# Kernel optimization log

Measured on AMD Instinct MI355X. Metric: run time of the kernel, lower is better.

## Reference

```python
import jax, jax.numpy as jnp
import numpy as np

N = 100000   # nodes
E = 1600000  # edges (avg degree 16)
D = 64       # feature dim (in_dim)


def setup_inputs() -> dict:
    key = jax.random.key(0)
    k1, k2, k3, k4, k5 = jax.random.split(key, 5)
    h = jax.random.normal(k1, (N, D), dtype=jnp.float32)
    dnorm = jax.random.uniform(k2, (N,), dtype=jnp.float32)  # deg^-1/2 proxy
    # xavier_normal_(gain=1.414) for Linear(2D, 1): std = gain*sqrt(2/(fan_in+fan_out))
    std = 1.414 * np.sqrt(2.0 / (2 * D + 1))
    gate_w = jax.random.normal(k3, (1, 2 * D), dtype=jnp.float32) * std
    gate_b = jnp.zeros((1,), dtype=jnp.float32)
    src = jax.random.randint(k4, (E,), 0, N, dtype=jnp.int32)
    dst = jax.random.randint(k5, (E,), 0, N, dtype=jnp.int32)
    return {"h": h, "dnorm": dnorm, "gate_w": gate_w, "gate_b": gate_b,
            "src": src, "dst": dst}


def reference(h, dnorm, gate_w, gate_b, src, dst):
    # gate(cat[h_dst, h_src]) == h_dst @ W[:, :D].T + h_src @ W[:, D:].T + b
    w_dst = gate_w[0, :D]  # [D]
    w_src = gate_w[0, D:]  # [D]
    h_src = h[src]                                        # [E, D] gather
    g = jnp.tanh(h[dst] @ w_dst + h_src @ w_src + gate_b[0])  # [E]
    e = g * dnorm[dst] * dnorm[src]                       # [E] (dropout p=0 -> identity)
    # u_mul_e + sum: z[v] = sum_{(u->v)} h[u] * e
    z = jax.ops.segment_sum(h_src * e[:, None], dst, num_segments=N)  # [N, D]
    return z
```

## Files before the change

### kernel.cpp

```cpp
#include <hip/hip_runtime.h>
#include <hip/hip_bf16.h>

#define D 64
#define BKT_SHIFT 7
#define BKT_NODES 128
#define NB_CNT 1024
#define DSPLIT_T 1024
#define DSPLIT_E 4096
#define CAP 2560

__device__ __forceinline__ unsigned short f2bf(float x) {
    unsigned u = __float_as_uint(x);
    unsigned r = 0x7fffu + ((u >> 16) & 1u);
    return (unsigned short)((u + r) >> 16);
}

template<bool MAKE_BF16>
__global__ void fal_precompute(const float* __restrict__ h,
                               const float* __restrict__ dnorm,
                               const float* __restrict__ gate_w,
                               const float* __restrict__ gate_b,
                               float2* __restrict__ sd,
                               float2* __restrict__ ss,
                               unsigned short* __restrict__ hb,
                               int N) {
    int tid  = threadIdx.x;
    int lane = tid & 63;
    int wave = tid >> 6;
    int grp  = lane >> 4;
    int gl   = lane & 15;

    int node = blockIdx.x * 16 + wave * 4 + grp;
    int nc   = node < N ? node : N - 1;

    const float4* h4 = (const float4*)h;
    const float4* w4 = (const float4*)gate_w;

    float4 hv  = h4[nc * 16 + gl];
    float4 wd  = w4[gl];
    float4 wsr = w4[16 + gl];

    if (MAKE_BF16 && node < N) {
        ushort4 p = make_ushort4(f2bf(hv.x), f2bf(hv.y), f2bf(hv.z), f2bf(hv.w));
        *(ushort4*)&hb[(size_t)node * D + gl * 4] = p;
    }

    float a = hv.x * wd.x + hv.y * wd.y + hv.z * wd.z + hv.w * wd.w;
    float b = hv.x * wsr.x + hv.y * wsr.y + hv.z * wsr.z + hv.w * wsr.w;

    for (int off = 1; off < 16; off <<= 1) {
        a += __shfl_xor(a, off, 64);
        b += __shfl_xor(b, off, 64);
    }

    if (gl == 0 && node < N) {
        float dn = dnorm[node];
        sd[node] = make_float2(a + gate_b[0], dn);
        ss[node] = make_float2(b, dn);
    }
}

__global__ __launch_bounds__(DSPLIT_T) void fal_multisplit(
        const int* __restrict__ src,
        const int* __restrict__ dst,
        int* __restrict__ bcursor,
        unsigned* __restrict__ pk_bin,
        int E, int nb) {
    __shared__ int lcount[NB_CNT];
    __shared__ int lscan[NB_CNT];
    __shared__ int gofs[NB_CNT];
    __shared__ int wsum16[16];
    __shared__ unsigned s_pk[DSPLIT_E];
    __shared__ int s_gpos[DSPLIT_E];

    int tid  = threadIdx.x;
    int lane = tid & 63;
    int w    = tid >> 6;
    lcount[tid] = 0;
    __syncthreads();

    int E4 = E >> 2;
    int i4 = blockIdx.x * DSPLIT_T + tid;

    int srcs[4], dsts[4], lr[4];
    bool act = (i4 < E4);
    if (act) {
        int4 s4 = ((const int4*)src)[i4];
        int4 d4 = ((const int4*)dst)[i4];
        srcs[0] = s4.x; srcs[1] = s4.y; srcs[2] = s4.z; srcs[3] = s4.w;
        dsts[0] = d4.x; dsts[1] = d4.y; dsts[2] = d4.z; dsts[3] = d4.w;
        #pragma unroll
        for (int j = 0; j < 4; ++j)
            lr[j] = atomicAdd(&lcount[dsts[j] >> BKT_SHIFT], 1);
    }
    __syncthreads();

    int v = lcount[tid];
    for (int off = 1; off < 64; off <<= 1) {
        int t = __shfl_up(v, off, 64);
        if (lane >= off) v += t;
    }
    if (lane == 63) wsum16[w] = v;
    __syncthreads();
    if (tid < 16) {
        int s = wsum16[tid];
        for (int off = 1; off < 16; off <<= 1) {
            int t = __shfl_up(s, off, 64);
            if (tid >= off) s += t;
        }
        wsum16[tid] = s;
    }
    __syncthreads();
    lscan[tid] = v + (w ? wsum16[w - 1] : 0);

    if (tid < nb) {
        int c = lcount[tid];
        int rel = c ? atomicAdd(&bcursor[tid], c) : 0;
        gofs[tid] = tid * CAP + rel;
    }
    __syncthreads();

    if (act) {
        #pragma unroll
        for (int j = 0; j < 4; ++j) {
            int b = dsts[j] >> BKT_SHIFT;
            int lpos = (lscan[b] - lcount[b]) + lr[j];
            unsigned dl = (unsigned)(dsts[j] & (BKT_NODES - 1));
            s_pk[lpos] = (dl << 20) | (unsigned)srcs[j];
            int gp = gofs[b] + lr[j];
            s_gpos[lpos] = (gp < (b + 1) * CAP) ? gp : -1;
        }
    }
    __syncthreads();

    int total = lscan[NB_CNT - 1];
    for (int t = tid; t < total; t += DSPLIT_T) {
        int g = s_gpos[t];
        if (g >= 0) pk_bin[g] = s_pk[t];
    }
}

template<bool BF16>
__global__ __launch_bounds__(512) void fal_bucket_process(
        const float* __restrict__ h,
        const unsigned short* __restrict__ hb,
        const float2* __restrict__ sd,
        const float2* __restrict__ ss,
        const int* __restrict__ bcursor,
        const unsigned* __restrict__ pk_bin,
        float* __restrict__ z, int N) {
    __shared__ unsigned s_pk[CAP];
    __shared__ unsigned s_srt[CAP];
    __shared__ float    s_esc[CAP];
    __shared__ float2   sdl[BKT_NODES];
    __shared__ int nhist[BKT_NODES];
    __shared__ int nbase[BKT_NODES];
    __shared__ int ncur[BKT_NODES];
    __shared__ int wsum8[8];

    int b    = blockIdx.x;
    int tid  = threadIdx.x;
    int lane = tid & 63;
    int w    = tid >> 6;

    if (tid < BKT_NODES) {
        nhist[tid] = 0;
        int node = b * BKT_NODES + tid;
        sdl[tid] = (node < N) ? sd[node] : make_float2(0.f, 0.f);
    }
    __syncthreads();

    int cnt = min(bcursor[b], CAP);
    const unsigned* bin = pk_bin + (size_t)b * CAP;

    for (int t = tid; t < cnt; t += 512) {
        unsigned pk = bin[t];
        s_pk[t] = pk;
        atomicAdd(&nhist[pk >> 20], 1);
    }
    __syncthreads();

    int myh = (tid < BKT_NODES) ? nhist[tid] : 0;
    int v = myh;
    for (int off = 1; off < 64; off <<= 1) {
        int t = __shfl_up(v, off, 64);
        if (lane >= off) v += t;
    }
    if (lane == 63) wsum8[w] = v;
    __syncthreads();
    if (tid < 8) {
        int s2 = wsum8[tid];
        for (int off = 1; off < 8; off <<= 1) {
            int t = __shfl_up(s2, off, 64);
            if (tid >= off) s2 += t;
        }
        wsum8[tid] = s2;
    }
    __syncthreads();
    if (tid < BKT_NODES) {
        int incl = v + (w ? wsum8[w - 1] : 0);
        nbase[tid] = incl - myh;
        ncur[tid]  = 0;
    }
    __syncthreads();

    for (int t = tid; t < cnt; t += 512) {
        unsigned pk = s_pk[t];
        int dl = (int)(pk >> 20);
        int sn = (int)(pk & 0xFFFFFu);
        int r  = atomicAdd(&ncur[dl], 1);
        float2 sv = ss[sn];
        float2 dv = sdl[dl];
        float esc = tanhf(dv.x + sv.x) * dv.y * sv.y;
        int p = nbase[dl] + r;
        s_srt[p] = pk;
        s_esc[p] = esc;
    }
    __syncthreads();

    int oct  = tid >> 3;
    int sdim = tid & 7;

    #pragma unroll
    for (int ni = 0; ni < BKT_NODES / 64; ++ni) {
        int dl   = oct + ni * 64;
        int seg0 = nbase[dl];
        int dg   = nhist[dl];

        float acc[8];
        #pragma unroll
        for (int i = 0; i < 8; ++i) acc[i] = 0.0f;

        int k = 0;
        for (; k + 2 <= dg; k += 2) {
            unsigned p0 = s_srt[seg0 + k];
            unsigned p1 = s_srt[seg0 + k + 1];
            float    e0 = s_esc[seg0 + k];
            float    e1 = s_esc[seg0 + k + 1];
            int s0 = (int)(p0 & 0xFFFFFu);
            int s1 = (int)(p1 & 0xFFFFFu);
            if (BF16) {
                uint4 a0 = *(const uint4*)&hb[(size_t)s0 * D + sdim * 8];
                uint4 a1 = *(const uint4*)&hb[(size_t)s1 * D + sdim * 8];
                acc[0] = fmaf(__uint_as_float(a0.x << 16),         e0, acc[0]);
                acc[1] = fmaf(__uint_as_float(a0.x & 0xffff0000u), e0, acc[1]);
                acc[2] = fmaf(__uint_as_float(a0.y << 16),         e0, acc[2]);
                acc[3] = fmaf(__uint_as_float(a0.y & 0xffff0000u), e0, acc[3]);
                acc[4] = fmaf(__uint_as_float(a0.z << 16),         e0, acc[4]);
                acc[5] = fmaf(__uint_as_float(a0.z & 0xffff0000u), e0, acc[5]);
                acc[6] = fmaf(__uint_as_float(a0.w << 16),         e0, acc[6]);
                acc[7] = fmaf(__uint_as_float(a0.w & 0xffff0000u), e0, acc[7]);
                acc[0] = fmaf(__uint_as_float(a1.x << 16),         e1, acc[0]);
                acc[1] = fmaf(__uint_as_float(a1.x & 0xffff0000u), e1, acc[1]);
                acc[2] = fmaf(__uint_as_float(a1.y << 16),         e1, acc[2]);
                acc[3] = fmaf(__uint_as_float(a1.y & 0xffff0000u), e1, acc[3]);
                acc[4] = fmaf(__uint_as_float(a1.z << 16),         e1, acc[4]);
                acc[5] = fmaf(__uint_as_float(a1.z & 0xffff0000u), e1, acc[5]);
                acc[6] = fmaf(__uint_as_float(a1.w << 16),         e1, acc[6]);
                acc[7] = fmaf(__uint_as_float(a1.w & 0xffff0000u), e1, acc[7]);
            } else {
                const float4* hp0 = (const float4*)&h[(size_t)s0 * D + sdim * 8];
                const float4* hp1 = (const float4*)&h[(size_t)s1 * D + sdim * 8];
                float4 q0 = hp0[0], q1 = hp0[1], q2 = hp1[0], q3 = hp1[1];
                acc[0] = fmaf(q0.x, e0, acc[0]); acc[1] = fmaf(q0.y, e0, acc[1]);
                acc[2] = fmaf(q0.z, e0, acc[2]); acc[3] = fmaf(q0.w, e0, acc[3]);
                acc[4] = fmaf(q1.x, e0, acc[4]); acc[5] = fmaf(q1.y, e0, acc[5]);
                acc[6] = fmaf(q1.z, e0, acc[6]); acc[7] = fmaf(q1.w, e0, acc[7]);
                acc[0] = fmaf(q2.x, e1, acc[0]); acc[1] = fmaf(q2.y, e1, acc[1]);
                acc[2] = fmaf(q2.z, e1, acc[2]); acc[3] = fmaf(q2.w, e1, acc[3]);
                acc[4] = fmaf(q3.x, e1, acc[4]); acc[5] = fmaf(q3.y, e1, acc[5]);
                acc[6] = fmaf(q3.z, e1, acc[6]); acc[7] = fmaf(q3.w, e1, acc[7]);
            }
        }
        if (k < dg) {
            unsigned p0 = s_srt[seg0 + k];
            float    e0 = s_esc[seg0 + k];
            int s0 = (int)(p0 & 0xFFFFFu);
            if (BF16) {
                uint4 a0 = *(const uint4*)&hb[(size_t)s0 * D + sdim * 8];
                acc[0] = fmaf(__uint_as_float(a0.x << 16),         e0, acc[0]);
                acc[1] = fmaf(__uint_as_float(a0.x & 0xffff0000u), e0, acc[1]);
                acc[2] = fmaf(__uint_as_float(a0.y << 16),         e0, acc[2]);
                acc[3] = fmaf(__uint_as_float(a0.y & 0xffff0000u), e0, acc[3]);
                acc[4] = fmaf(__uint_as_float(a0.z << 16),         e0, acc[4]);
                acc[5] = fmaf(__uint_as_float(a0.z & 0xffff0000u), e0, acc[5]);
                acc[6] = fmaf(__uint_as_float(a0.w << 16),         e0, acc[6]);
                acc[7] = fmaf(__uint_as_float(a0.w & 0xffff0000u), e0, acc[7]);
            } else {
                const float4* hp0 = (const float4*)&h[(size_t)s0 * D + sdim * 8];
                float4 q0 = hp0[0], q1 = hp0[1];
                acc[0] = fmaf(q0.x, e0, acc[0]); acc[1] = fmaf(q0.y, e0, acc[1]);
                acc[2] = fmaf(q0.z, e0, acc[2]); acc[3] = fmaf(q0.w, e0, acc[3]);
                acc[4] = fmaf(q1.x, e0, acc[4]); acc[5] = fmaf(q1.y, e0, acc[5]);
                acc[6] = fmaf(q1.z, e0, acc[6]); acc[7] = fmaf(q1.w, e0, acc[7]);
            }
        }

        int node = b * BKT_NODES + dl;
        if (node < N) {
            float4* zp = (float4*)&z[(size_t)node * D + sdim * 8];
            zp[0] = make_float4(acc[0], acc[1], acc[2], acc[3]);
            zp[1] = make_float4(acc[4], acc[5], acc[6], acc[7]);
        }
    }
}

extern "C" void kernel_launch(void* const* d_in, const int* in_sizes, int n_in,
                              void* d_out, int out_size, void* d_ws, size_t ws_size,
                              hipStream_t stream) {
    const float* h      = (const float*)d_in[0];
    const float* dnorm  = (const float*)d_in[1];
    const float* gate_w = (const float*)d_in[2];
    const float* gate_b = (const float*)d_in[3];
    const int*   src    = (const int*)d_in[4];
    const int*   dst    = (const int*)d_in[5];
    float*       z      = (float*)d_out;

    int N  = in_sizes[1];
    int E  = in_sizes[4];
    int nb = (N + BKT_NODES - 1) >> BKT_SHIFT;

    char* ws0 = (char*)d_ws;
    size_t off = 0;
    auto alloc = [&](size_t bytes) {
        char* p = ws0 + off;
        off += (bytes + 15) & ~(size_t)15;
        return p;
    };
    float2*   sd      = (float2*)alloc((size_t)N * sizeof(float2));
    float2*   ss      = (float2*)alloc((size_t)N * sizeof(float2));
    int*      bcursor = (int*)alloc((size_t)nb * sizeof(int));
    unsigned* pk_bin  = (unsigned*)alloc((size_t)nb * CAP * sizeof(unsigned));
    unsigned short* hb = (unsigned short*)(ws0 + off);
    size_t need_with_hb = off + (size_t)N * D * sizeof(unsigned short);
    bool use_bf16 = (ws_size >= need_with_hb);

    hipMemsetAsync(bcursor, 0, (size_t)nb * sizeof(int), stream);

    if (use_bf16)
        fal_precompute<true><<<(N + 15) / 16, 256, 0, stream>>>(
            h, dnorm, gate_w, gate_b, sd, ss, hb, N);
    else
        fal_precompute<false><<<(N + 15) / 16, 256, 0, stream>>>(
            h, dnorm, gate_w, gate_b, sd, ss, hb, N);

    fal_multisplit<<<(E + DSPLIT_E - 1) / DSPLIT_E, DSPLIT_T, 0, stream>>>(
        src, dst, bcursor, pk_bin, E, nb);

    if (use_bf16)
        fal_bucket_process<true><<<nb, 512, 0, stream>>>(
            h, hb, sd, ss, bcursor, pk_bin, z, N);
    else
        fal_bucket_process<false><<<nb, 512, 0, stream>>>(
            h, hb, sd, ss, bcursor, pk_bin, z, N);
}
```

Measured before the change: 169.7 us.

## Make bucket processing persistent with atomic work queue, pack sorted edges, unroll by four

```diff
diff --git a/kernel.cpp b/kernel.cpp
--- a/kernel.cpp
+++ b/kernel.cpp
@@ -148,160 +148,196 @@
         const float2* __restrict__ ss,
         const int* __restrict__ bcursor,
         const unsigned* __restrict__ pk_bin,
-        float* __restrict__ z, int N) {
+        int* __restrict__ wcur,
+        float* __restrict__ z, int N, int nb) {
     __shared__ unsigned s_pk[CAP];
-    __shared__ unsigned s_srt[CAP];
-    __shared__ float    s_esc[CAP];
+    __shared__ uint2    s_sorted[CAP];
     __shared__ float2   sdl[BKT_NODES];
     __shared__ int nhist[BKT_NODES];
     __shared__ int nbase[BKT_NODES];
     __shared__ int ncur[BKT_NODES];
     __shared__ int wsum8[8];
-
-    int b    = blockIdx.x;
+    __shared__ int s_b;
+
     int tid  = threadIdx.x;
     int lane = tid & 63;
     int w    = tid >> 6;
-
-    if (tid < BKT_NODES) {
-        nhist[tid] = 0;
-        int node = b * BKT_NODES + tid;
-        sdl[tid] = (node < N) ? sd[node] : make_float2(0.f, 0.f);
-    }
-    __syncthreads();
-
-    int cnt = min(bcursor[b], CAP);
-    const unsigned* bin = pk_bin + (size_t)b * CAP;
-
-    for (int t = tid; t < cnt; t += 512) {
-        unsigned pk = bin[t];
-        s_pk[t] = pk;
-        atomicAdd(&nhist[pk >> 20], 1);
-    }
-    __syncthreads();
-
-    int myh = (tid < BKT_NODES) ? nhist[tid] : 0;
-    int v = myh;
-    for (int off = 1; off < 64; off <<= 1) {
-        int t = __shfl_up(v, off, 64);
-        if (lane >= off) v += t;
-    }
-    if (lane == 63) wsum8[w] = v;
-    __syncthreads();
-    if (tid < 8) {
-        int s2 = wsum8[tid];
-        for (int off = 1; off < 8; off <<= 1) {
-            int t = __shfl_up(s2, off, 64);
-            if (tid >= off) s2 += t;
-        }
-        wsum8[tid] = s2;
-    }
-    __syncthreads();
-    if (tid < BKT_NODES) {
-        int incl = v + (w ? wsum8[w - 1] : 0);
-        nbase[tid] = incl - myh;
-        ncur[tid]  = 0;
-    }
-    __syncthreads();
-
-    for (int t = tid; t < cnt; t += 512) {
-        unsigned pk = s_pk[t];
-        int dl = (int)(pk >> 20);
-        int sn = (int)(pk & 0xFFFFFu);
-        int r  = atomicAdd(&ncur[dl], 1);
-        float2 sv = ss[sn];
-        float2 dv = sdl[dl];
-        float esc = tanhf(dv.x + sv.x) * dv.y * sv.y;
-        int p = nbase[dl] + r;
-        s_srt[p] = pk;
-        s_esc[p] = esc;
-    }
-    __syncthreads();
-
     int oct  = tid >> 3;
     int sdim = tid & 7;
 
-    #pragma unroll
-    for (int ni = 0; ni < BKT_NODES / 64; ++ni) {
-        int dl   = oct + ni * 64;
-        int seg0 = nbase[dl];
-        int dg   = nhist[dl];
-
-        float acc[8];
+    for (;;) {
+        if (tid == 0) s_b = atomicAdd(wcur, 1);
+        __syncthreads();
+        int b = s_b;
+        if (b >= nb) return;
+
+        if (tid < BKT_NODES) {
+            nhist[tid] = 0;
+            int node = b * BKT_NODES + tid;
+            sdl[tid] = (node < N) ? sd[node] : make_float2(0.f, 0.f);
+        }
+        __syncthreads();
+
+        int cnt = min(bcursor[b], CAP);
+        const unsigned* bin = pk_bin + (size_t)b * CAP;
+
+        for (int t = tid; t < cnt; t += 512) {
+            unsigned pk = bin[t];
+            s_pk[t] = pk;
+            atomicAdd(&nhist[pk >> 20], 1);
+        }
+        __syncthreads();
+
+        int myh = (tid < BKT_NODES) ? nhist[tid] : 0;
+        int v = myh;
+        for (int off = 1; off < 64; off <<= 1) {
+            int t = __shfl_up(v, off, 64);
+            if (lane >= off) v += t;
+        }
+        if (lane == 63) wsum8[w] = v;
+        __syncthreads();
+        if (tid < 8) {
+            int s2 = wsum8[tid];
+            for (int off = 1; off < 8; off <<= 1) {
+                int t = __shfl_up(s2, off, 64);
+                if (tid >= off) s2 += t;
+            }
+            wsum8[tid] = s2;
+        }
+        __syncthreads();
+        if (tid < BKT_NODES) {
+            int incl = v + (w ? wsum8[w - 1] : 0);
+            nbase[tid] = incl - myh;
+            ncur[tid]  = 0;
+        }
+        __syncthreads();
+
+        for (int t = tid; t < cnt; t += 512) {
+            unsigned pk = s_pk[t];
+            int dl = (int)(pk >> 20);
+            int sn = (int)(pk & 0xFFFFFu);
+            int r  = atomicAdd(&ncur[dl], 1);
+            float2 sv = ss[sn];
+            float2 dv = sdl[dl];
+            float esc = tanhf(dv.x + sv.x) * dv.y * sv.y;
+            s_sorted[nbase[dl] + r] = make_uint2(pk, __float_as_uint(esc));
+        }
+        __syncthreads();
+
         #pragma unroll
-        for (int i = 0; i < 8; ++i) acc[i] = 0.0f;
-
-        int k = 0;
-        for (; k + 2 <= dg; k += 2) {
-            unsigned p0 = s_srt[seg0 + k];
-            unsigned p1 = s_srt[seg0 + k + 1];
-            float    e0 = s_esc[seg0 + k];
-            float    e1 = s_esc[seg0 + k + 1];
-            int s0 = (int)(p0 & 0xFFFFFu);
-            int s1 = (int)(p1 & 0xFFFFFu);
-            if (BF16) {
-                uint4 a0 = *(const uint4*)&hb[(size_t)s0 * D + sdim * 8];
-                uint4 a1 = *(const uint4*)&hb[(size_t)s1 * D + sdim * 8];
-                acc[0] = fmaf(__uint_as_float(a0.x << 16),         e0, acc[0]);
-                acc[1] = fmaf(__uint_as_float(a0.x & 0xffff0000u), e0, acc[1]);
-                acc[2] = fmaf(__uint_as_float(a0.y << 16),         e0, acc[2]);
-                acc[3] = fmaf(__uint_as_float(a0.y & 0xffff0000u), e0, acc[3]);
-                acc[4] = fmaf(__uint_as_float(a0.z << 16),         e0, acc[4]);
-                acc[5] = fmaf(__uint_as_float(a0.z & 0xffff0000u), e0, acc[5]);
-                acc[6] = fmaf(__uint_as_float(a0.w << 16),         e0, acc[6]);
-                acc[7] = fmaf(__uint_as_float(a0.w & 0xffff0000u), e0, acc[7]);
-                acc[0] = fmaf(__uint_as_float(a1.x << 16),         e1, acc[0]);
-                acc[1] = fmaf(__uint_as_float(a1.x & 0xffff0000u), e1, acc[1]);
-                acc[2] = fmaf(__uint_as_float(a1.y << 16),         e1, acc[2]);
-                acc[3] = fmaf(__uint_as_float(a1.y & 0xffff0000u), e1, acc[3]);
-                acc[4] = fmaf(__uint_as_float(a1.z << 16),         e1, acc[4]);
-                acc[5] = fmaf(__uint_as_float(a1.z & 0xffff0000u), e1, acc[5]);
-                acc[6] = fmaf(__uint_as_float(a1.w << 16),         e1, acc[6]);
-                acc[7] = fmaf(__uint_as_float(a1.w & 0xffff0000u), e1, acc[7]);
-            } else {
-                const float4* hp0 = (const float4*)&h[(size_t)s0 * D + sdim * 8];
-                const float4* hp1 = (const float4*)&h[(size_t)s1 * D + sdim * 8];
-                float4 q0 = hp0[0], q1 = hp0[1], q2 = hp1[0], q3 = hp1[1];
-                acc[0] = fmaf(q0.x, e0, acc[0]); acc[1] = fmaf(q0.y, e0, acc[1]);
-                acc[2] = fmaf(q0.z, e0, acc[2]); acc[3] = fmaf(q0.w, e0, acc[3]);
-                acc[4] = fmaf(q1.x, e0, acc[4]); acc[5] = fmaf(q1.y, e0, acc[5]);
-                acc[6] = fmaf(q1.z, e0, acc[6]); acc[7] = fmaf(q1.w, e0, acc[7]);
-                acc[0] = fmaf(q2.x, e1, acc[0]); acc[1] = fmaf(q2.y, e1, acc[1]);
-                acc[2] = fmaf(q2.z, e1, acc[2]); acc[3] = fmaf(q2.w, e1, acc[3]);
-                acc[4] = fmaf(q3.x, e1, acc[4]); acc[5] = fmaf(q3.y, e1, acc[5]);
-                acc[6] = fmaf(q3.z, e1, acc[6]); acc[7] = fmaf(q3.w, e1, acc[7]);
+        for (int ni = 0; ni < BKT_NODES / 64; ++ni) {
+            int dl   = oct + ni * 64;
+            int seg0 = nbase[dl];
+            int dg   = nhist[dl];
+
+            float acc[8];
+            #pragma unroll
+            for (int i = 0; i < 8; ++i) acc[i] = 0.0f;
+
+            int k = 0;
+            for (; k + 4 <= dg; k += 4) {
+                uint2 r0 = s_sorted[seg0 + k];
+                uint2 r1 = s_sorted[seg0 + k + 1];
+                uint2 r2 = s_sorted[seg0 + k + 2];
+                uint2 r3 = s_sorted[seg0 + k + 3];
+                int s0 = (int)(r0.x & 0xFFFFFu), s1 = (int)(r1.x & 0xFFFFFu);
+                int s2 = (int)(r2.x & 0xFFFFFu), s3 = (int)(r3.x & 0xFFFFFu);
+                float e0 = __uint_as_float(r0.y), e1 = __uint_as_float(r1.y);
+                float e2 = __uint_as_float(r2.y), e3 = __uint_as_float(r3.y);
+                if (BF16) {
+                    uint4 a0 = *(const uint4*)&hb[(size_t)s0 * D + sdim * 8];
+                    uint4 a1 = *(const uint4*)&hb[(size_t)s1 * D + sdim * 8];
+                    uint4 a2 = *(const uint4*)&hb[(size_t)s2 * D + sdim * 8];
+                    uint4 a3 = *(const uint4*)&hb[(size_t)s3 * D + sdim * 8];
+                    acc[0] = fmaf(__uint_as_float(a0.x << 16),         e0, acc[0]);
+                    acc[1] = fmaf(__uint_as_float(a0.x & 0xffff0000u), e0, acc[1]);
+                    acc[2] = fmaf(__uint_as_float(a0.y << 16),         e0, acc[2]);
+                    acc[3] = fmaf(__uint_as_float(a0.y & 0xffff0000u), e0, acc[3]);
+                    acc[4] = fmaf(__uint_as_float(a0.z << 16),         e0, acc[4]);
+                    acc[5] = fmaf(__uint_as_float(a0.z & 0xffff0000u), e0, acc[5]);
+                    acc[6] = fmaf(__uint_as_float(a0.w << 16),         e0, acc[6]);
+                    acc[7] = fmaf(__uint_as_float(a0.w & 0xffff0000u), e0, acc[7]);
+                    acc[0] = fmaf(__uint_as_float(a1.x << 16),         e1, acc[0]);
+                    acc[1] = fmaf(__uint_as_float(a1.x & 0xffff0000u), e1, acc[1]);
+                    acc[2] = fmaf(__uint_as_float(a1.y << 16),         e1, acc[2]);
+                    acc[3] = fmaf(__uint_as_float(a1.y & 0xffff0000u), e1, acc[3]);
+                    acc[4] = fmaf(__uint_as_float(a1.z << 16),         e1, acc[4]);
+                    acc[5] = fmaf(__uint_as_float(a1.z & 0xffff0000u), e1, acc[5]);
+                    acc[6] = fmaf(__uint_as_float(a1.w << 16),         e1, acc[6]);
+                    acc[7] = fmaf(__uint_as_float(a1.w & 0xffff0000u), e1, acc[7]);
+                    acc[0] = fmaf(__uint_as_float(a2.x << 16),         e2, acc[0]);
+                    acc[1] = fmaf(__uint_as_float(a2.x & 0xffff0000u), e2, acc[1]);
+                    acc[2] = fmaf(__uint_as_float(a2.y << 16),         e2, acc[2]);
+                    acc[3] = fmaf(__uint_as_float(a2.y & 0xffff0000u), e2, acc[3]);
+                    acc[4] = fmaf(__uint_as_float(a2.z << 16),         e2, acc[4]);
+                    acc[5] = fmaf(__uint_as_float(a2.z & 0xffff0000u), e2, acc[5]);
+                    acc[6] = fmaf(__uint_as_float(a2.w << 16),         e2, acc[6]);
+                    acc[7] = fmaf(__uint_as_float(a2.w & 0xffff0000u), e2, acc[7]);
+                    acc[0] = fmaf(__uint_as_float(a3.x << 16),         e3, acc[0]);
+                    acc[1] = fmaf(__uint_as_float(a3.x & 0xffff0000u), e3, acc[1]);
+                    acc[2] = fmaf(__uint_as_float(a3.y << 16),         e3, acc[2]);
+                    acc[3] = fmaf(__uint_as_float(a3.y & 0xffff0000u), e3, acc[3]);
+                    acc[4] = fmaf(__uint_as_float(a3.z << 16),         e3, acc[4]);
+                    acc[5] = fmaf(__uint_as_float(a3.z & 0xffff0000u), e3, acc[5]);
+                    acc[6] = fmaf(__uint_as_float(a3.w << 16),         e3, acc[6]);
+                    acc[7] = fmaf(__uint_as_float(a3.w & 0xffff0000u), e3, acc[7]);
+                } else {
+                    const float4* p0 = (const float4*)&h[(size_t)s0 * D + sdim * 8];
+                    const float4* p1 = (const float4*)&h[(size_t)s1 * D + sdim * 8];
+                    const float4* p2 = (const float4*)&h[(size_t)s2 * D + sdim * 8];
+                    const float4* p3 = (const float4*)&h[(size_t)s3 * D + sdim * 8];
+                    float4 q0 = p0[0], q1 = p0[1], q2 = p1[0], q3 = p1[1];
+                    float4 q4 = p2[0], q5 = p2[1], q6 = p3[0], q7 = p3[1];
+                    acc[0] = fmaf(q0.x, e0, acc[0]); acc[1] = fmaf(q0.y, e0, acc[1]);
+                    acc[2] = fmaf(q0.z, e0, acc[2]); acc[3] = fmaf(q0.w, e0, acc[3]);
+                    acc[4] = fmaf(q1.x, e0, acc[4]); acc[5] = fmaf(q1.y, e0, acc[5]);
+                    acc[6] = fmaf(q1.z, e0, acc[6]); acc[7] = fmaf(q1.w, e0, acc[7]);
+                    acc[0] = fmaf(q2.x, e1, acc[0]); acc[1] = fmaf(q2.y, e1, acc[1]);
+                    acc[2] = fmaf(q2.z, e1, acc[2]); acc[3] = fmaf(q2.w, e1, acc[3]);
+                    acc[4] = fmaf(q3.x, e1, acc[4]); acc[5] = fmaf(q3.y, e1, acc[5]);
+                    acc[6] = fmaf(q3.z, e1, acc[6]); acc[7] = fmaf(q3.w, e1, acc[7]);
+                    acc[0] = fmaf(q4.x, e2, acc[0]); acc[1] = fmaf(q4.y, e2, acc[1]);
+                    acc[2] = fmaf(q4.z, e2, acc[2]); acc[3] = fmaf(q4.w, e2, acc[3]);
+                    acc[4] = fmaf(q5.x, e2, acc[4]); acc[5] = fmaf(q5.y, e2, acc[5]);
+                    acc[6] = fmaf(q5.z, e2, acc[6]); acc[7] = fmaf(q5.w, e2, acc[7]);
+                    acc[0] = fmaf(q6.x, e3, acc[0]); acc[1] = fmaf(q6.y, e3, acc[1]);
+                    acc[2] = fmaf(q6.z, e3, acc[2]); acc[3] = fmaf(q6.w, e3, acc[3]);
+                    acc[4] = fmaf(q7.x, e3, acc[4]); acc[5] = fmaf(q7.y, e3, acc[5]);
+                    acc[6] = fmaf(q7.z, e3, acc[6]); acc[7] = fmaf(q7.w, e3, acc[7]);
+                }
             }
-        }
-        if (k < dg) {
-            unsigned p0 = s_srt[seg0 + k];
-            float    e0 = s_esc[seg0 + k];
-            int s0 = (int)(p0 & 0xFFFFFu);
-            if (BF16) {
-                uint4 a0 = *(const uint4*)&hb[(size_t)s0 * D + sdim * 8];
-                acc[0] = fmaf(__uint_as_float(a0.x << 16),         e0, acc[0]);
-                acc[1] = fmaf(__uint_as_float(a0.x & 0xffff0000u), e0, acc[1]);
-                acc[2] = fmaf(__uint_as_float(a0.y << 16),         e0, acc[2]);
-                acc[3] = fmaf(__uint_as_float(a0.y & 0xffff0000u), e0, acc[3]);
-                acc[4] = fmaf(__uint_as_float(a0.z << 16),         e0, acc[4]);
-                acc[5] = fmaf(__uint_as_float(a0.z & 0xffff0000u), e0, acc[5]);
-                acc[6] = fmaf(__uint_as_float(a0.w << 16),         e0, acc[6]);
-                acc[7] = fmaf(__uint_as_float(a0.w & 0xffff0000u), e0, acc[7]);
-            } else {
-                const float4* hp0 = (const float4*)&h[(size_t)s0 * D + sdim * 8];
-                float4 q0 = hp0[0], q1 = hp0[1];
-                acc[0] = fmaf(q0.x, e0, acc[0]); acc[1] = fmaf(q0.y, e0, acc[1]);
-                acc[2] = fmaf(q0.z, e0, acc[2]); acc[3] = fmaf(q0.w, e0, acc[3]);
-                acc[4] = fmaf(q1.x, e0, acc[4]); acc[5] = fmaf(q1.y, e0, acc[5]);
-                acc[6] = fmaf(q1.z, e0, acc[6]); acc[7] = fmaf(q1.w, e0, acc[7]);
+            for (; k < dg; ++k) {
+                uint2 r0 = s_sorted[seg0 + k];
+                int s0 = (int)(r0.x & 0xFFFFFu);
+                float e0 = __uint_as_float(r0.y);
+                if (BF16) {
+                    uint4 a0 = *(const uint4*)&hb[(size_t)s0 * D + sdim * 8];
+                    acc[0] = fmaf(__uint_as_float(a0.x << 16),         e0, acc[0]);
+                    acc[1] = fmaf(__uint_as_float(a0.x & 0xffff0000u), e0, acc[1]);
+                    acc[2] = fmaf(__uint_as_float(a0.y << 16),         e0, acc[2]);
+                    acc[3] = fmaf(__uint_as_float(a0.y & 0xffff0000u), e0, acc[3]);
+                    acc[4] = fmaf(__uint_as_float(a0.z << 16),         e0, acc[4]);
+                    acc[5] = fmaf(__uint_as_float(a0.z & 0xffff0000u), e0, acc[5]);
+                    acc[6] = fmaf(__uint_as_float(a0.w << 16),         e0, acc[6]);
+                    acc[7] = fmaf(__uint_as_float(a0.w & 0xffff0000u), e0, acc[7]);
+                } else {
+                    const float4* p0 = (const float4*)&h[(size_t)s0 * D + sdim * 8];
+                    float4 q0 = p0[0], q1 = p0[1];
+                    acc[0] = fmaf(q0.x, e0, acc[0]); acc[1] = fmaf(q0.y, e0, acc[1]);
+                    acc[2] = fmaf(q0.z, e0, acc[2]); acc[3] = fmaf(q0.w, e0, acc[3]);
+                    acc[4] = fmaf(q1.x, e0, acc[4]); acc[5] = fmaf(q1.y, e0, acc[5]);
+                    acc[6] = fmaf(q1.z, e0, acc[6]); acc[7] = fmaf(q1.w, e0, acc[7]);
+                }
             }
-        }
-
-        int node = b * BKT_NODES + dl;
-        if (node < N) {
-            float4* zp = (float4*)&z[(size_t)node * D + sdim * 8];
-            zp[0] = make_float4(acc[0], acc[1], acc[2], acc[3]);
-            zp[1] = make_float4(acc[4], acc[5], acc[6], acc[7]);
-        }
+
+            int node = b * BKT_NODES + dl;
+            if (node < N) {
+                float4* zp = (float4*)&z[(size_t)node * D + sdim * 8];
+                zp[0] = make_float4(acc[0], acc[1], acc[2], acc[3]);
+                zp[1] = make_float4(acc[4], acc[5], acc[6], acc[7]);
+            }
+        }
+        __syncthreads();
     }
 }
 
@@ -330,12 +366,13 @@
     float2*   sd      = (float2*)alloc((size_t)N * sizeof(float2));
     float2*   ss      = (float2*)alloc((size_t)N * sizeof(float2));
     int*      bcursor = (int*)alloc((size_t)nb * sizeof(int));
+    int*      wcur    = (int*)alloc(16);
     unsigned* pk_bin  = (unsigned*)alloc((size_t)nb * CAP * sizeof(unsigned));
     unsigned short* hb = (unsigned short*)(ws0 + off);
     size_t need_with_hb = off + (size_t)N * D * sizeof(unsigned short);
     bool use_bf16 = (ws_size >= need_with_hb);
 
-    hipMemsetAsync(bcursor, 0, (size_t)nb * sizeof(int), stream);
+    hipMemsetAsync(bcursor, 0, (size_t)((char*)(wcur + 4) - (char*)bcursor), stream);
 
     if (use_bf16)
         fal_precompute<true><<<(N + 15) / 16, 256, 0, stream>>>(
@@ -347,10 +384,11 @@
     fal_multisplit<<<(E + DSPLIT_E - 1) / DSPLIT_E, DSPLIT_T, 0, stream>>>(
         src, dst, bcursor, pk_bin, E, nb);
 
+    int pgrid = 1024;
     if (use_bf16)
-        fal_bucket_process<true><<<nb, 512, 0, stream>>>(
-            h, hb, sd, ss, bcursor, pk_bin, z, N);
+        fal_bucket_process<true><<<pgrid, 512, 0, stream>>>(
+            h, hb, sd, ss, bcursor, pk_bin, wcur, z, N, nb);
     else
-        fal_bucket_process<false><<<nb, 512, 0, stream>>>(
-            h, hb, sd, ss, bcursor, pk_bin, z, N);
-}
+        fal_bucket_process<false><<<pgrid, 512, 0, stream>>>(
+            h, hb, sd, ss, bcursor, pk_bin, wcur, z, N, nb);
+}
```

Result: slower. 175.7 us (+3.6%).
